# Performance work log

Measured on AMD Instinct MI355X. Metric: run time of the kernel, lower is better.

## Reference

```python
import jax, jax.numpy as jnp
import numpy as np

B, H, L, DH = 4, 16, 2048, 64
EMBED_DIM = H * DH
CAUSAL = True


def setup_inputs() -> dict:
    key = jax.random.key(0)
    kq, kk, kv = jax.random.split(key, 3)
    return {
        "query": jax.random.normal(kq, (B, H, L, DH), dtype=jnp.float32),
        "key": jax.random.normal(kk, (B, H, L, DH), dtype=jnp.float32),
        "value": jax.random.normal(kv, (B, H, L, DH), dtype=jnp.float32),
    }


def reference(query, key, value):
    # scaled dot-product attention with causal mask, inputs [B, H, L, Dh]
    scale = 1.0 / jnp.sqrt(jnp.asarray(query.shape[-1], query.dtype))
    scores = jnp.einsum("bhld,bhsd->bhls", query, key) * scale  # [B,H,L,S]
    if CAUSAL:
        q_idx = jnp.arange(query.shape[-2])[:, None]
        k_idx = jnp.arange(key.shape[-2])[None, :]
        neg_inf = jnp.asarray(-jnp.inf, scores.dtype)
        scores = jnp.where(k_idx > q_idx, neg_inf, scores)
    attn = jax.nn.softmax(scores, axis=-1)
    out = jnp.einsum("bhls,bhsd->bhld", attn, value)  # [B,H,L,Dh]
    # merge heads -> [B, L, D]
    b = out.shape[0]
    return out.transpose(0, 2, 1, 3).reshape(b, -1, EMBED_DIM)
```

## Files before the change

kernel.cpp:

```cpp
#include <hip/hip_runtime.h>
#include <hip/hip_bf16.h>

#define B_   4
#define H_   16
#define L_   2048
#define DH_  64
#define QSCALE 0.1803368801111204f
#define LDK  72

typedef __bf16 bf16;
typedef __bf16 bf16x4 __attribute__((ext_vector_type(4)));
typedef __bf16 bf16x8 __attribute__((ext_vector_type(8)));
typedef float  f32x4  __attribute__((ext_vector_type(4)));

typedef const __attribute__((address_space(1))) unsigned int* gptr_t;
typedef __attribute__((address_space(3))) unsigned int* lptr_t;

__device__ __forceinline__ void load_lds16(const bf16* g, bf16* l) {
    __builtin_amdgcn_global_load_lds((gptr_t)(const void*)g, (lptr_t)(void*)l, 16, 0, 0);
}

__global__ __launch_bounds__(256, 4)
void prep(const float* __restrict__ K, const float* __restrict__ V,
          bf16* __restrict__ Kb, bf16* __restrict__ Vtg)
{
    __shared__ bf16 tl[64 * 72];
    const int t   = threadIdx.x;
    const int r   = t >> 2;
    const int c4  = t & 3;
    const int bid = blockIdx.x;
    const int kt  = bid & 31;
    const int bh  = bid >> 5;

    const float* Kp = K + ((size_t)bh * L_ + kt * 64) * DH_;
    const float* Vp = V + ((size_t)bh * L_ + kt * 64) * DH_;
    bf16* Kbp = Kb  + (size_t)bh * (L_ * DH_) + (size_t)(kt * 64) * DH_;
    bf16* Vtp = Vtg + (size_t)bh * (DH_ * L_) + kt * 64;

    {
        const float* src = Kp + r * DH_ + c4 * 16;
        f32x4 a = *(const f32x4*)(src);
        f32x4 b = *(const f32x4*)(src + 4);
        f32x4 c = *(const f32x4*)(src + 8);
        f32x4 d = *(const f32x4*)(src + 12);
        bf16x8 lo, hi;
        #pragma unroll
        for (int j = 0; j < 4; ++j) {
            lo[j] = (bf16)a[j]; lo[j + 4] = (bf16)b[j];
            hi[j] = (bf16)c[j]; hi[j + 4] = (bf16)d[j];
        }
        const int b0 = 2 * c4, b1 = 2 * c4 + 1;
        *(bf16x8*)(Kbp + r * 64 + (b0 ^ (r & 7)) * 8) = lo;
        *(bf16x8*)(Kbp + r * 64 + (b1 ^ (r & 7)) * 8) = hi;
    }
    {
        const float* src = Vp + r * DH_ + c4 * 16;
        f32x4 a = *(const f32x4*)(src);
        f32x4 b = *(const f32x4*)(src + 4);
        f32x4 c = *(const f32x4*)(src + 8);
        f32x4 d = *(const f32x4*)(src + 12);
        #pragma unroll
        for (int j = 0; j < 4; ++j) {
            tl[(c4 * 16 + j)      * 72 + r] = (bf16)a[j];
            tl[(c4 * 16 + 4 + j)  * 72 + r] = (bf16)b[j];
            tl[(c4 * 16 + 8 + j)  * 72 + r] = (bf16)c[j];
            tl[(c4 * 16 + 12 + j) * 72 + r] = (bf16)d[j];
        }
    }
    __syncthreads();
    {
        const int d = r;
        #pragma unroll
        for (int bi = 0; bi < 2; ++bi) {
            const int blk = 2 * c4 + bi;
            bf16x8 v;
            #pragma unroll
            for (int j = 0; j < 8; ++j) v[j] = tl[d * 72 + blk * 8 + j];
            *(bf16x8*)(Vtp + (size_t)d * L_ + (blk ^ (d & 7)) * 8) = v;
        }
    }
}

__global__ __launch_bounds__(256, 4)
void fa_fwd2(const float* __restrict__ Q, const bf16* __restrict__ Kb,
             const bf16* __restrict__ Vtg, float* __restrict__ O)
{
    __shared__ __align__(16) bf16 smem[2][2][64 * 64];
    __shared__ __align__(16) bf16 Pl[4][16 * 64];

    const int tid  = threadIdx.x;
    const int wave = tid >> 6;
    const int lane = tid & 63;
    const int quad = lane >> 4;
    const int l15  = lane & 15;

    const int u    = blockIdx.x;
    const int xcd  = u & 7;
    const int p    = u >> 3;
    const int bh   = xcd * 8 + (p & 7);
    const int pidx = p >> 3;
    const int h    = bh & 15;
    const int b    = bh >> 4;

    const float* Qbh = Q + (size_t)bh * L_ * DH_;
    const bf16* Kbh  = Kb  + (size_t)bh * (L_ * DH_);
    const bf16* Vbh  = Vtg + (size_t)bh * (DH_ * L_);

    const int Rw = 16 * wave;
    const int lr = lane >> 3;
    const int lb = lane & 7;

    bf16x8 vone;
    #pragma unroll
    for (int jj = 0; jj < 8; ++jj) vone[jj] = (bf16)1.0f;

    int swb[2];
    #pragma unroll
    for (int s = 0; s < 2; ++s) swb[s] = ((4 * s + quad) ^ (l15 & 7)) * 8;

    #pragma unroll
    for (int pass = 0; pass < 2; ++pass) {
        const int qt = pass ? (31 - pidx) : pidx;
        const int q0 = qt * 64;

        bf16x8 qf[2];
        {
            const int row = q0 + Rw + l15;
            const float* qp = Qbh + (size_t)row * DH_ + quad * 8;
            #pragma unroll
            for (int s = 0; s < 2; ++s) {
                f32x4 a = *(const f32x4*)(qp + s * 32);
                f32x4 c = *(const f32x4*)(qp + s * 32 + 4);
                #pragma unroll
                for (int jj = 0; jj < 4; ++jj) {
                    qf[s][jj]     = (bf16)(a[jj] * QSCALE);
                    qf[s][jj + 4] = (bf16)(c[jj] * QSCALE);
                }
            }
        }

        f32x4 o_acc[4];
        f32x4 l_acc = (f32x4)0.0f;
        #pragma unroll
        for (int ct = 0; ct < 4; ++ct) o_acc[ct] = (f32x4)0.0f;

        {
            const bf16* kg = Kbh + (size_t)(q0 * 0 + Rw + lr) * 64 + lb * 8;
            const bf16* vg = Vbh + (size_t)(Rw + lr) * L_ + lb * 8;
            bf16* kl = &smem[0][0][Rw * 64];
            bf16* vl = &smem[0][1][Rw * 64];
            load_lds16(kg, kl);              load_lds16(kg + 8 * 64, kl + 8 * 64);
            load_lds16(vg, vl);              load_lds16(vg + (size_t)8 * L_, vl + 8 * 64);
        }

        for (int j = 0; j <= qt; ++j) {
            __syncthreads();
            const int cur = j & 1;

            if (j < qt) {
                const int nb  = cur ^ 1;
                const int kv0 = (j + 1) * 64;
                const bf16* kg = Kbh + (size_t)(kv0 + Rw + lr) * 64 + lb * 8;
                const bf16* vg = Vbh + (size_t)(Rw + lr) * L_ + kv0 + lb * 8;
                bf16* kl = &smem[nb][0][Rw * 64];
                bf16* vl = &smem[nb][1][Rw * 64];
                load_lds16(kg, kl);          load_lds16(kg + 8 * 64, kl + 8 * 64);
                load_lds16(vg, vl);          load_lds16(vg + (size_t)8 * L_, vl + 8 * 64);
            }

            const bf16* Kl = smem[cur][0];
            const bf16* Vt = smem[cur][1];

            f32x4 sacc[4];
            #pragma unroll
            for (int ct = 0; ct < 4; ++ct) {
                f32x4 acc = (f32x4)0.0f;
                #pragma unroll
                for (int s = 0; s < 2; ++s) {
                    bf16x8 bk = *(const bf16x8*)&Kl[(16 * ct + l15) * 64 + swb[s]];
                    acc = __builtin_amdgcn_mfma_f32_16x16x32_bf16(qf[s], bk, acc, 0, 0, 0);
                }
                sacc[ct] = acc;
            }

            if (j == qt) {
                #pragma unroll
                for (int ct = 0; ct < 4; ++ct) {
                    const int keyl = 16 * ct + l15;
                    #pragma unroll
                    for (int r = 0; r < 4; ++r)
                        if (keyl > Rw + quad * 4 + r) sacc[ct][r] = -1e30f;
                }
            }

            #pragma unroll
            for (int ct = 0; ct < 4; ++ct)
                #pragma unroll
                for (int r = 0; r < 4; ++r)
                    sacc[ct][r] = exp2f(sacc[ct][r]);

            #pragma unroll
            for (int ct = 0; ct < 4; ++ct)
                #pragma unroll
                for (int r = 0; r < 4; ++r) {
                    const int q = quad * 4 + r;
                    const int c = 2 * ct + (l15 >> 3);
                    Pl[wave][q * 64 + ((c ^ (q & 7)) * 8) + (l15 & 7)] = (bf16)sacc[ct][r];
                }
            bf16x8 pa[2];
            #pragma unroll
            for (int s = 0; s < 2; ++s)
                pa[s] = *(const bf16x8*)&Pl[wave][l15 * 64 + swb[s]];

            #pragma unroll
            for (int ct = 0; ct < 4; ++ct)
                #pragma unroll
                for (int s = 0; s < 2; ++s) {
                    bf16x8 bv = *(const bf16x8*)&Vt[(16 * ct + l15) * 64 + swb[s]];
                    o_acc[ct] = __builtin_amdgcn_mfma_f32_16x16x32_bf16(pa[s], bv, o_acc[ct], 0, 0, 0);
                }
            #pragma unroll
            for (int s = 0; s < 2; ++s)
                l_acc = __builtin_amdgcn_mfma_f32_16x16x32_bf16(pa[s], vone, l_acc, 0, 0, 0);
        }
        __syncthreads();

        #pragma unroll
        for (int r = 0; r < 4; ++r) {
            const float inv = 1.0f / l_acc[r];
            const int qrow = q0 + Rw + quad * 4 + r;
            float* op = &O[((size_t)b * L_ + qrow) * (H_ * DH_) + h * DH_];
            #pragma unroll
            for (int ct = 0; ct < 4; ++ct)
                op[16 * ct + l15] = o_acc[ct][r] * inv;
        }
    }
}

__global__ __launch_bounds__(256, 4)
void fa_fwd(const float* __restrict__ Q, const float* __restrict__ K,
            const float* __restrict__ V, float* __restrict__ O)
{
    __shared__ __align__(16) bf16 Kl[64 * LDK];
    __shared__ __align__(16) bf16 Vt[64 * LDK];
    __shared__ __align__(16) bf16 Pl[4][16 * LDK];

    const int tid  = threadIdx.x;
    const int wave = tid >> 6;
    const int lane = tid & 63;
    const int quad = lane >> 4;
    const int l15  = lane & 15;

    const int u    = blockIdx.x;
    const int xcd  = u & 7;
    const int p    = u >> 3;
    const int bh   = xcd * 8 + (p & 7);
    const int pidx = p >> 3;
    const int h    = bh & 15;
    const int b    = bh >> 4;

    const float* Qbh = Q + (size_t)bh * L_ * DH_;
    const float* Kbh = K + (size_t)bh * L_ * DH_;
    const float* Vbh = V + (size_t)bh * L_ * DH_;

    const int r0 = tid >> 4;
    const int c0 = (tid & 15) * 4;

    #pragma unroll
    for (int pass = 0; pass < 2; ++pass) {
        const int qt = pass ? (31 - pidx) : pidx;
        const int q0 = qt * 64;

        bf16x8 qf[2];
        {
            const int row = q0 + wave * 16 + l15;
            const float* qp = Qbh + (size_t)row * DH_ + quad * 8;
            #pragma unroll
            for (int s = 0; s < 2; ++s) {
                f32x4 a = *(const f32x4*)(qp + s * 32);
                f32x4 c = *(const f32x4*)(qp + s * 32 + 4);
                #pragma unroll
                for (int jj = 0; jj < 4; ++jj) {
                    qf[s][jj]     = (bf16)(a[jj] * QSCALE);
                    qf[s][jj + 4] = (bf16)(c[jj] * QSCALE);
                }
            }
        }

        float m_run[4], l_run[4];
        f32x4 o_acc[4];
        #pragma unroll
        for (int r = 0; r < 4; ++r) { m_run[r] = -1e30f; l_run[r] = 0.0f; }
        #pragma unroll
        for (int ct = 0; ct < 4; ++ct) o_acc[ct] = (f32x4)0.0f;

        f32x4 kreg[4], vreg[4];
        #pragma unroll
        for (int i = 0; i < 4; ++i) {
            kreg[i] = *(const f32x4*)(Kbh + (size_t)(r0 + 16 * i) * DH_ + c0);
            vreg[i] = *(const f32x4*)(Vbh + (size_t)(r0 + 16 * i) * DH_ + c0);
        }

        for (int j = 0; j <= qt; ++j) {
            __syncthreads();
            #pragma unroll
            for (int i = 0; i < 4; ++i) {
                const int row = r0 + 16 * i;
                bf16x4 kb;
                #pragma unroll
                for (int c = 0; c < 4; ++c) kb[c] = (bf16)kreg[i][c];
                *(bf16x4*)&Kl[row * LDK + c0] = kb;
                Vt[(c0 + 0) * LDK + row] = (bf16)vreg[i][0];
                Vt[(c0 + 1) * LDK + row] = (bf16)vreg[i][1];
                Vt[(c0 + 2) * LDK + row] = (bf16)vreg[i][2];
                Vt[(c0 + 3) * LDK + row] = (bf16)vreg[i][3];
            }
            __syncthreads();

            if (j < qt) {
                const int kv0 = (j + 1) * 64;
                #pragma unroll
                for (int i = 0; i < 4; ++i) {
                    kreg[i] = *(const f32x4*)(Kbh + (size_t)(kv0 + r0 + 16 * i) * DH_ + c0);
                    vreg[i] = *(const f32x4*)(Vbh + (size_t)(kv0 + r0 + 16 * i) * DH_ + c0);
                }
            }

            f32x4 sacc[4];
            #pragma unroll
            for (int ct = 0; ct < 4; ++ct) {
                f32x4 acc = (f32x4)0.0f;
                #pragma unroll
                for (int s = 0; s < 2; ++s) {
                    bf16x8 bk = *(const bf16x8*)&Kl[(16 * ct + l15) * LDK + 32 * s + quad * 8];
                    acc = __builtin_amdgcn_mfma_f32_16x16x32_bf16(qf[s], bk, acc, 0, 0, 0);
                }
                sacc[ct] = acc;
            }

            if (j == qt) {
                #pragma unroll
                for (int ct = 0; ct < 4; ++ct) {
                    const int keyl = 16 * ct + l15;
                    #pragma unroll
                    for (int r = 0; r < 4; ++r)
                        if (keyl > wave * 16 + quad * 4 + r) sacc[ct][r] = -1e30f;
                }
            }

            #pragma unroll
            for (int r = 0; r < 4; ++r) {
                float mx = fmaxf(fmaxf(sacc[0][r], sacc[1][r]), fmaxf(sacc[2][r], sacc[3][r]));
                mx = fmaxf(mx, __shfl_xor(mx, 1));
                mx = fmaxf(mx, __shfl_xor(mx, 2));
                mx = fmaxf(mx, __shfl_xor(mx, 4));
                mx = fmaxf(mx, __shfl_xor(mx, 8));
                const float mnew  = fmaxf(m_run[r], mx);
                const float alpha = exp2f(m_run[r] - mnew);
                float sum = 0.0f;
                #pragma unroll
                for (int ct = 0; ct < 4; ++ct) {
                    const float pv = exp2f(sacc[ct][r] - mnew);
                    sacc[ct][r] = pv;
                    sum += pv;
                }
                sum += __shfl_xor(sum, 1);
                sum += __shfl_xor(sum, 2);
                sum += __shfl_xor(sum, 4);
                sum += __shfl_xor(sum, 8);
                l_run[r] = l_run[r] * alpha + sum;
                m_run[r] = mnew;
                #pragma unroll
                for (int ct = 0; ct < 4; ++ct) o_acc[ct][r] *= alpha;
            }

            #pragma unroll
            for (int ct = 0; ct < 4; ++ct)
                #pragma unroll
                for (int r = 0; r < 4; ++r)
                    Pl[wave][(quad * 4 + r) * LDK + 16 * ct + l15] = (bf16)sacc[ct][r];

            bf16x8 pa[2];
            #pragma unroll
            for (int s = 0; s < 2; ++s)
                pa[s] = *(const bf16x8*)&Pl[wave][l15 * LDK + 32 * s + quad * 8];

            #pragma unroll
            for (int ct = 0; ct < 4; ++ct)
                #pragma unroll
                for (int s = 0; s < 2; ++s) {
                    bf16x8 bv = *(const bf16x8*)&Vt[(16 * ct + l15) * LDK + 32 * s + quad * 8];
                    o_acc[ct] = __builtin_amdgcn_mfma_f32_16x16x32_bf16(pa[s], bv, o_acc[ct], 0, 0, 0);
                }
        }

        #pragma unroll
        for (int ct = 0; ct < 4; ++ct)
            #pragma unroll
            for (int r = 0; r < 4; ++r) {
                const int qrow = q0 + wave * 16 + quad * 4 + r;
                O[((size_t)b * L_ + qrow) * (H_ * DH_) + h * DH_ + (16 * ct + l15)] =
                    o_acc[ct][r] / l_run[r];
            }
    }
}

extern "C" void kernel_launch(void* const* d_in, const int* in_sizes, int n_in,
                              void* d_out, int out_size, void* d_ws, size_t ws_size,
                              hipStream_t stream) {
    const float* q = (const float*)d_in[0];
    const float* k = (const float*)d_in[1];
    const float* v = (const float*)d_in[2];
    float* out = (float*)d_out;
    const size_t need = 2ull * (size_t)(B_ * H_) * L_ * DH_ * sizeof(bf16);
    if (ws_size >= need) {
        bf16* Kb  = (bf16*)d_ws;
        bf16* Vtg = Kb + (size_t)(B_ * H_) * L_ * DH_;
        prep<<<dim3(B_ * H_ * (L_ / 64)), dim3(256), 0, stream>>>(k, v, Kb, Vtg);
        fa_fwd2<<<dim3(B_ * H_ * 16), dim3(256), 0, stream>>>(q, Kb, Vtg, out);
    } else {
        fa_fwd<<<dim3(B_ * H_ * 16), dim3(256), 0, stream>>>(q, k, v, out);
    }
}
```

Measured before the change: 197.4 us.

## Process 128-row query tiles per block with two query groups per wave

The attention kernel now has each wave handle 32 query rows as two 16-row groups. K fragments are loaded from LDS once per tile and reused for both groups, and each V fragment feeds two MFMAs. The QK product is computed transposed so that P can be written to LDS as packed 4-wide stores. The grid is halved to 512 blocks and the launch bound lowered to 2 blocks per SM, so the kernel trades occupancy and register pressure for less LDS traffic and fewer global K/V tile loads per query row.

```diff
diff --git a/kernel.cpp b/kernel.cpp
--- a/kernel.cpp
+++ b/kernel.cpp
@@ -81,8 +81,8 @@
     }
 }
 
-__global__ __launch_bounds__(256, 4)
-void fa_fwd2(const float* __restrict__ Q, const bf16* __restrict__ Kb,
+__global__ __launch_bounds__(256, 2)
+void fa_fwd3(const float* __restrict__ Q, const bf16* __restrict__ Kb,
              const bf16* __restrict__ Vtg, float* __restrict__ O)
 {
     __shared__ __align__(16) bf16 smem[2][2][64 * 64];
@@ -96,9 +96,10 @@
 
     const int u    = blockIdx.x;
     const int xcd  = u & 7;
-    const int p    = u >> 3;
-    const int bh   = xcd * 8 + (p & 7);
-    const int pidx = p >> 3;
+    const int t    = u >> 3;
+    const int bh   = xcd * 8 + (t & 7);
+    const int pidx = t >> 3;
+
     const int h    = bh & 15;
     const int b    = bh >> 4;
 
@@ -118,14 +119,15 @@
     #pragma unroll
     for (int s = 0; s < 2; ++s) swb[s] = ((4 * s + quad) ^ (l15 & 7)) * 8;
 
-    #pragma unroll
     for (int pass = 0; pass < 2; ++pass) {
-        const int qt = pass ? (31 - pidx) : pidx;
-        const int q0 = qt * 64;
-
-        bf16x8 qf[2];
-        {
-            const int row = q0 + Rw + l15;
+        const int Qt  = pass ? (15 - pidx) : pidx;
+        const int q0  = Qt * 128;
+        const int jmax = 2 * Qt + 1;
+
+        bf16x8 qf[2][2];
+        #pragma unroll
+        for (int qg = 0; qg < 2; ++qg) {
+            const int row = q0 + 32 * wave + 16 * qg + l15;
             const float* qp = Qbh + (size_t)row * DH_ + quad * 8;
             #pragma unroll
             for (int s = 0; s < 2; ++s) {
@@ -133,19 +135,23 @@
                 f32x4 c = *(const f32x4*)(qp + s * 32 + 4);
                 #pragma unroll
                 for (int jj = 0; jj < 4; ++jj) {
-                    qf[s][jj]     = (bf16)(a[jj] * QSCALE);
-                    qf[s][jj + 4] = (bf16)(c[jj] * QSCALE);
-                }
-            }
-        }
-
-        f32x4 o_acc[4];
-        f32x4 l_acc = (f32x4)0.0f;
-        #pragma unroll
-        for (int ct = 0; ct < 4; ++ct) o_acc[ct] = (f32x4)0.0f;
+                    qf[qg][s][jj]     = (bf16)(a[jj] * QSCALE);
+                    qf[qg][s][jj + 4] = (bf16)(c[jj] * QSCALE);
+                }
+            }
+        }
+
+        f32x4 o_acc[2][4];
+        f32x4 l_acc[2];
+        #pragma unroll
+        for (int qg = 0; qg < 2; ++qg) {
+            l_acc[qg] = (f32x4)0.0f;
+            #pragma unroll
+            for (int ct = 0; ct < 4; ++ct) o_acc[qg][ct] = (f32x4)0.0f;
+        }
 
         {
-            const bf16* kg = Kbh + (size_t)(q0 * 0 + Rw + lr) * 64 + lb * 8;
+            const bf16* kg = Kbh + (size_t)(Rw + lr) * 64 + lb * 8;
             const bf16* vg = Vbh + (size_t)(Rw + lr) * L_ + lb * 8;
             bf16* kl = &smem[0][0][Rw * 64];
             bf16* vl = &smem[0][1][Rw * 64];
@@ -153,11 +159,11 @@
             load_lds16(vg, vl);              load_lds16(vg + (size_t)8 * L_, vl + 8 * 64);
         }
 
-        for (int j = 0; j <= qt; ++j) {
+        for (int j = 0; j <= jmax; ++j) {
             __syncthreads();
             const int cur = j & 1;
 
-            if (j < qt) {
+            if (j < jmax) {
                 const int nb  = cur ^ 1;
                 const int kv0 = (j + 1) * 64;
                 const bf16* kg = Kbh + (size_t)(kv0 + Rw + lr) * 64 + lb * 8;
@@ -171,69 +177,78 @@
             const bf16* Kl = smem[cur][0];
             const bf16* Vt = smem[cur][1];
 
-            f32x4 sacc[4];
+            bf16x8 bk[4][2];
+            #pragma unroll
+            for (int ct = 0; ct < 4; ++ct)
+                #pragma unroll
+                for (int s = 0; s < 2; ++s)
+                    bk[ct][s] = *(const bf16x8*)&Kl[(16 * ct + l15) * 64 + swb[s]];
+
+            bf16x8 pa[2][2];
+            #pragma unroll
+            for (int qg = 0; qg < 2; ++qg) {
+                f32x4 sacc[4];
+                #pragma unroll
+                for (int ct = 0; ct < 4; ++ct) {
+                    f32x4 acc = (f32x4)0.0f;
+                    #pragma unroll
+                    for (int s = 0; s < 2; ++s)
+                        acc = __builtin_amdgcn_mfma_f32_16x16x32_bf16(bk[ct][s], qf[qg][s], acc, 0, 0, 0);
+                    sacc[ct] = acc;
+                }
+
+                if (j >= 2 * Qt) {
+                    const int rlim = 32 * wave + 16 * qg + l15 - ((j - 2 * Qt) << 6);
+                    #pragma unroll
+                    for (int ct = 0; ct < 4; ++ct) {
+                        #pragma unroll
+                        for (int r = 0; r < 4; ++r)
+                            if (16 * ct + quad * 4 + r > rlim) sacc[ct][r] = -1e30f;
+                    }
+                }
+
+                #pragma unroll
+                for (int ct = 0; ct < 4; ++ct) {
+                    bf16x4 pk;
+                    #pragma unroll
+                    for (int r = 0; r < 4; ++r) pk[r] = (bf16)exp2f(sacc[ct][r]);
+                    const int blk = 2 * ct + (quad >> 1);
+                    *(bf16x4*)&Pl[wave][l15 * 64 + ((blk ^ (l15 & 7)) * 8) + (quad & 1) * 4] = pk;
+                }
+                #pragma unroll
+                for (int s = 0; s < 2; ++s)
+                    pa[qg][s] = *(const bf16x8*)&Pl[wave][l15 * 64 + swb[s]];
+            }
+
             #pragma unroll
             for (int ct = 0; ct < 4; ++ct) {
-                f32x4 acc = (f32x4)0.0f;
-                #pragma unroll
-                for (int s = 0; s < 2; ++s) {
-                    bf16x8 bk = *(const bf16x8*)&Kl[(16 * ct + l15) * 64 + swb[s]];
-                    acc = __builtin_amdgcn_mfma_f32_16x16x32_bf16(qf[s], bk, acc, 0, 0, 0);
-                }
-                sacc[ct] = acc;
-            }
-
-            if (j == qt) {
-                #pragma unroll
-                for (int ct = 0; ct < 4; ++ct) {
-                    const int keyl = 16 * ct + l15;
-                    #pragma unroll
-                    for (int r = 0; r < 4; ++r)
-                        if (keyl > Rw + quad * 4 + r) sacc[ct][r] = -1e30f;
-                }
-            }
-
-            #pragma unroll
-            for (int ct = 0; ct < 4; ++ct)
-                #pragma unroll
-                for (int r = 0; r < 4; ++r)
-                    sacc[ct][r] = exp2f(sacc[ct][r]);
-
-            #pragma unroll
-            for (int ct = 0; ct < 4; ++ct)
-                #pragma unroll
-                for (int r = 0; r < 4; ++r) {
-                    const int q = quad * 4 + r;
-                    const int c = 2 * ct + (l15 >> 3);
-                    Pl[wave][q * 64 + ((c ^ (q & 7)) * 8) + (l15 & 7)] = (bf16)sacc[ct][r];
-                }
-            bf16x8 pa[2];
-            #pragma unroll
-            for (int s = 0; s < 2; ++s)
-                pa[s] = *(const bf16x8*)&Pl[wave][l15 * 64 + swb[s]];
-
-            #pragma unroll
-            for (int ct = 0; ct < 4; ++ct)
                 #pragma unroll
                 for (int s = 0; s < 2; ++s) {
                     bf16x8 bv = *(const bf16x8*)&Vt[(16 * ct + l15) * 64 + swb[s]];
-                    o_acc[ct] = __builtin_amdgcn_mfma_f32_16x16x32_bf16(pa[s], bv, o_acc[ct], 0, 0, 0);
-                }
-            #pragma unroll
-            for (int s = 0; s < 2; ++s)
-                l_acc = __builtin_amdgcn_mfma_f32_16x16x32_bf16(pa[s], vone, l_acc, 0, 0, 0);
+                    #pragma unroll
+                    for (int qg = 0; qg < 2; ++qg)
+                        o_acc[qg][ct] = __builtin_amdgcn_mfma_f32_16x16x32_bf16(pa[qg][s], bv, o_acc[qg][ct], 0, 0, 0);
+                }
+            }
+            #pragma unroll
+            for (int qg = 0; qg < 2; ++qg)
+                #pragma unroll
+                for (int s = 0; s < 2; ++s)
+                    l_acc[qg] = __builtin_amdgcn_mfma_f32_16x16x32_bf16(pa[qg][s], vone, l_acc[qg], 0, 0, 0);
         }
         __syncthreads();
 
         #pragma unroll
-        for (int r = 0; r < 4; ++r) {
-            const float inv = 1.0f / l_acc[r];
-            const int qrow = q0 + Rw + quad * 4 + r;
-            float* op = &O[((size_t)b * L_ + qrow) * (H_ * DH_) + h * DH_];
-            #pragma unroll
-            for (int ct = 0; ct < 4; ++ct)
-                op[16 * ct + l15] = o_acc[ct][r] * inv;
-        }
+        for (int qg = 0; qg < 2; ++qg)
+            #pragma unroll
+            for (int r = 0; r < 4; ++r) {
+                const float inv = 1.0f / l_acc[qg][r];
+                const int qrow = q0 + 32 * wave + 16 * qg + quad * 4 + r;
+                float* op = &O[((size_t)b * L_ + qrow) * (H_ * DH_) + h * DH_];
+                #pragma unroll
+                for (int ct = 0; ct < 4; ++ct)
+                    op[16 * ct + l15] = o_acc[qg][ct][r] * inv;
+            }
     }
 }
 
@@ -266,7 +281,6 @@
     const int r0 = tid >> 4;
     const int c0 = (tid & 15) * 4;
 
-    #pragma unroll
     for (int pass = 0; pass < 2; ++pass) {
         const int qt = pass ? (31 - pidx) : pidx;
         const int q0 = qt * 64;
@@ -417,7 +431,7 @@
         bf16* Kb  = (bf16*)d_ws;
         bf16* Vtg = Kb + (size_t)(B_ * H_) * L_ * DH_;
         prep<<<dim3(B_ * H_ * (L_ / 64)), dim3(256), 0, stream>>>(k, v, Kb, Vtg);
-        fa_fwd2<<<dim3(B_ * H_ * 16), dim3(256), 0, stream>>>(q, Kb, Vtg, out);
+        fa_fwd3<<<dim3(512), dim3(256), 0, stream>>>(q, Kb, Vtg, out);
     } else {
         fa_fwd<<<dim3(B_ * H_ * 16), dim3(256), 0, stream>>>(q, k, v, out);
     }
```

Measured after the change: 190.4 us. -3.6%, faster.
